# Optimization experiments

Hardware: AMD Instinct MI355X
Metric: run time of the kernel (lower is better)

Reference implementation:

```python
import jax, jax.numpy as jnp
import numpy as np

B, T, E, H, K = 256, 512, 768, 100, 11
START, STOP = 9, 10
NEG = -1000.0


def setup_inputs() -> dict:
    key = jax.random.key(0)
    ks = jax.random.split(key, 12)
    s = 0.1
    Hd = H // 2  # per-direction hidden (bidirectional)
    trans = jax.random.normal(ks[9], (K, K), jnp.float32)
    trans = trans.at[:, START].set(NEG).at[STOP, :].set(NEG)
    return {
        "embeddings": jax.random.normal(ks[0], (B, T, E), jnp.float32),
        "input_mask": jnp.ones((B, T), jnp.int32),
        "W_ih_f": jax.random.normal(ks[1], (4 * Hd, E), jnp.float32) * s,
        "W_hh_f": jax.random.normal(ks[2], (4 * Hd, Hd), jnp.float32) * s,
        "b_f": jax.random.normal(ks[3], (4 * Hd,), jnp.float32) * s,
        "W_ih_b": jax.random.normal(ks[4], (4 * Hd, E), jnp.float32) * s,
        "W_hh_b": jax.random.normal(ks[5], (4 * Hd, Hd), jnp.float32) * s,
        "b_b": jax.random.normal(ks[6], (4 * Hd,), jnp.float32) * s,
        "W_out": jax.random.normal(ks[7], (K, H), jnp.float32) * s,
        "b_out": jax.random.normal(ks[8], (K,), jnp.float32) * s,
        "transitions": trans,
    }


def _lstm_dir(x, W_ih, W_hh, b, reverse):
    # x: [B, T, E] -> hidden states [B, T, Hd]; zero initial state.
    Bn = x.shape[0]
    Hd = W_hh.shape[1]

    def step(carry, xt):
        h, c = carry
        g = xt @ W_ih.T + h @ W_hh.T + b  # [B, 4*Hd], torch gate order i,f,g,o
        i, f, gg, o = jnp.split(g, 4, axis=-1)
        c = jax.nn.sigmoid(f) * c + jax.nn.sigmoid(i) * jnp.tanh(gg)
        h = jax.nn.sigmoid(o) * jnp.tanh(c)
        return (h, c), h

    init = (jnp.zeros((Bn, Hd), x.dtype), jnp.zeros((Bn, Hd), x.dtype))
    _, hs = jax.lax.scan(step, init, jnp.swapaxes(x, 0, 1), reverse=reverse)
    return jnp.swapaxes(hs, 0, 1)


def _emissions(embeddings, W_ih_f, W_hh_f, b_f, W_ih_b, W_hh_b, b_b, W_out, b_out):
    h_f = _lstm_dir(embeddings, W_ih_f, W_hh_f, b_f, reverse=False)
    h_b = _lstm_dir(embeddings, W_ih_b, W_hh_b, b_b, reverse=True)
    lstm_out = jnp.concatenate([h_f, h_b], axis=-1)  # [B, T, H]
    return lstm_out @ W_out.T + b_out  # [B, T, K]


def reference(embeddings, input_mask, W_ih_f, W_hh_f, b_f, W_ih_b, W_hh_b, b_b,
              W_out, b_out, transitions):
    logits = _emissions(embeddings, W_ih_f, W_hh_f, b_f, W_ih_b, W_hh_b, b_b,
                        W_out, b_out)  # [B, T, K]
    Bn = logits.shape[0]
    mask = (input_mask > 0)

    alpha0 = jnp.full((Bn, K), NEG, logits.dtype).at[:, START].set(0.0)
    idK = jnp.arange(K, dtype=jnp.int32)

    def step(alpha, inp):
        frame, m = inp  # frame [B,K], m [B] bool
        # smat[b, prev, cur] = alpha[b,prev] + frame[b,cur] + trans[prev,cur]
        smat = alpha[:, :, None] + frame[:, None, :] + transitions[None]
        bp = jnp.argmax(smat, axis=1).astype(jnp.int32)          # [B, K]
        new_alpha = jax.nn.logsumexp(smat, axis=1)               # [B, K]
        alpha = jnp.where(m[:, None], new_alpha, alpha)
        bp = jnp.where(m[:, None], bp, idK[None, :])
        return alpha, bp

    alpha_T, bps = jax.lax.scan(
        step, alpha0,
        (jnp.swapaxes(logits, 0, 1), jnp.swapaxes(mask, 0, 1)))  # bps [T,B,K]

    final = alpha_T + transitions[None, :, STOP]                 # [B, K]
    scores = jax.nn.logsumexp(final, axis=1)                     # [B]
    best = jnp.argmax(final, axis=1).astype(jnp.int32)           # [B]

    bidx = jnp.arange(Bn)

    def back(cur, bp_t):
        prev = bp_t[bidx, cur]
        return prev, prev

    # Original skips backtrace[0]; backtrack over positions 1..T-1.
    _, path_prefix = jax.lax.scan(back, best, bps[1:], reverse=True)  # [T-1, B]
    paths = jnp.concatenate(
        [jnp.swapaxes(path_prefix, 0, 1), best[:, None]], axis=1)     # [B, T]
    return scores, paths
```

## Files before the change

### kernel.cpp

```cpp
#include <hip/hip_runtime.h>
#include <math.h>


typedef _Float16 half8 __attribute__((ext_vector_type(8)));
typedef _Float16 half4 __attribute__((ext_vector_type(4)));
typedef float f32x4 __attribute__((ext_vector_type(4)));

__global__ __launch_bounds__(256) void k_gemm_split(
    const float* __restrict__ emb,
    const float* __restrict__ Wf,
    const float* __restrict__ Wb,
    float* __restrict__ xw)
{
    __shared__ _Float16 Ah[128 * 64];
    __shared__ _Float16 Al[128 * 64];
    __shared__ _Float16 Bh[80 * 64];
    __shared__ _Float16 Bl[80 * 64];

    const int bid = blockIdx.x;
    const int wg  = (bid & 7) * 640 + (bid >> 3);
    const int mt  = wg / 5;
    const int nb  = wg - mt * 5;
    const size_t m0 = (size_t)mt * 128;
    const int n0 = nb * 80;

    const int tid  = threadIdx.x;
    const int lane = tid & 63;
    const int w    = tid >> 6;
    const int grp  = lane >> 4;
    const int r16  = lane & 15;

    f32x4 acc[2][5];
    #pragma unroll
    for (int m = 0; m < 2; ++m)
        #pragma unroll
        for (int n = 0; n < 5; ++n) acc[m][n] = (f32x4){0.f, 0.f, 0.f, 0.f};

    for (int kt = 0; kt < 12; ++kt) {
        const int k0 = kt * 64;
        __syncthreads();

        #pragma unroll
        for (int j = 0; j < 8; ++j) {
            const int flat = j * 256 + tid;
            const int row  = flat >> 4;
            const int q    = flat & 15;
            const float4 v = *(const float4*)(emb + (m0 + row) * 768 + k0 + q * 4);
            half4 hv, lv;
            hv[0] = (_Float16)v.x; lv[0] = (_Float16)(v.x - (float)hv[0]);
            hv[1] = (_Float16)v.y; lv[1] = (_Float16)(v.y - (float)hv[1]);
            hv[2] = (_Float16)v.z; lv[2] = (_Float16)(v.z - (float)hv[2]);
            hv[3] = (_Float16)v.w; lv[3] = (_Float16)(v.w - (float)hv[3]);
            const int s    = (q >> 1) ^ (row & 7);
            const int addr = row * 64 + s * 8 + (q & 1) * 4;
            *(half4*)(Ah + addr) = hv;
            *(half4*)(Al + addr) = lv;
        }
        #pragma unroll
        for (int j = 0; j < 5; ++j) {
            const int flat = j * 256 + tid;
            const int row  = flat >> 4;
            const int q    = flat & 15;
            const int n    = n0 + row;
            const float* src = (n < 200) ? (Wf + (size_t)n * 768)
                                         : (Wb + (size_t)(n - 200) * 768);
            const float4 v = *(const float4*)(src + k0 + q * 4);
            half4 hv, lv;
            hv[0] = (_Float16)v.x; lv[0] = (_Float16)(v.x - (float)hv[0]);
            hv[1] = (_Float16)v.y; lv[1] = (_Float16)(v.y - (float)hv[1]);
            hv[2] = (_Float16)v.z; lv[2] = (_Float16)(v.z - (float)hv[2]);
            hv[3] = (_Float16)v.w; lv[3] = (_Float16)(v.w - (float)hv[3]);
            const int s    = (q >> 1) ^ (row & 7);
            const int addr = row * 64 + s * 8 + (q & 1) * 4;
            *(half4*)(Bh + addr) = hv;
            *(half4*)(Bl + addr) = lv;
        }
        __syncthreads();

        #pragma unroll
        for (int ks = 0; ks < 2; ++ks) {
            const int kslot = ks * 4 + grp;
            half8 ah[2], al[2], bh[5], bl[5];
            #pragma unroll
            for (int m = 0; m < 2; ++m) {
                const int row = w * 32 + m * 16 + r16;
                const int ad  = row * 64 + (kslot ^ (row & 7)) * 8;
                ah[m] = *(half8*)(Ah + ad);
                al[m] = *(half8*)(Al + ad);
            }
            #pragma unroll
            for (int n = 0; n < 5; ++n) {
                const int row = n * 16 + r16;
                const int ad  = row * 64 + (kslot ^ (row & 7)) * 8;
                bh[n] = *(half8*)(Bh + ad);
                bl[n] = *(half8*)(Bl + ad);
            }
            #pragma unroll
            for (int m = 0; m < 2; ++m)
                #pragma unroll
                for (int n = 0; n < 5; ++n) {
                    acc[m][n] = __builtin_amdgcn_mfma_f32_16x16x32_f16(ah[m], bh[n], acc[m][n], 0, 0, 0);
                    acc[m][n] = __builtin_amdgcn_mfma_f32_16x16x32_f16(ah[m], bl[n], acc[m][n], 0, 0, 0);
                    acc[m][n] = __builtin_amdgcn_mfma_f32_16x16x32_f16(al[m], bh[n], acc[m][n], 0, 0, 0);
                }
        }
    }

    #pragma unroll
    for (int m = 0; m < 2; ++m) {
        #pragma unroll
        for (int n = 0; n < 5; ++n) {
            #pragma unroll
            for (int i = 0; i < 4; ++i) {
                const size_t row = m0 + w * 32 + m * 16 + (lane >> 4) * 4 + i;
                const int    col = n0 + n * 16 + (lane & 15);
                xw[row * 400 + col] = acc[m][n][i];
            }
        }
    }
}

__global__ __launch_bounds__(256) void k_lstm(
    const float* __restrict__ xw,
    const float* __restrict__ Whh_f,
    const float* __restrict__ Whh_b,
    const float* __restrict__ bf_,
    const float* __restrict__ bb_,
    float* __restrict__ hout)
{
    const int b   = blockIdx.x >> 1;
    const int dir = blockIdx.x & 1;
    const int g   = threadIdx.x;

    __shared__ float h_s[52];
    __shared__ float g_s[200];

    const float* Whh  = dir ? Whh_b : Whh_f;
    const float* bias = dir ? bb_ : bf_;

    float w[52];
    float bg = 0.f;
    if (g < 200) {
        #pragma unroll
        for (int j = 0; j < 50; ++j) w[j] = Whh[g * 50 + j];
        w[50] = 0.f; w[51] = 0.f;
        bg = bias[g];
    } else {
        #pragma unroll
        for (int j = 0; j < 52; ++j) w[j] = 0.f;
    }

    if (g < 52) h_s[g] = 0.f;
    float c = 0.f;
    __syncthreads();

    const size_t base = (size_t)b * 512;

    float xv = 0.f;
    {
        int t0 = dir ? 511 : 0;
        if (g < 200) xv = xw[(base + t0) * 400 + dir * 200 + g];
    }

    for (int it = 0; it < 512; ++it) {
        const int t = dir ? (511 - it) : it;
        float xcur = xv;
        if (it + 1 < 512) {
            int tn = dir ? (510 - it) : (it + 1);
            if (g < 200) xv = xw[(base + tn) * 400 + dir * 200 + g];
        }

        float sum = bg + xcur;
        const float4* h4 = (const float4*)h_s;
        #pragma unroll
        for (int q = 0; q < 13; ++q) {
            float4 hv = h4[q];
            sum = fmaf(w[q * 4 + 0], hv.x, sum);
            sum = fmaf(w[q * 4 + 1], hv.y, sum);
            sum = fmaf(w[q * 4 + 2], hv.z, sum);
            sum = fmaf(w[q * 4 + 3], hv.w, sum);
        }
        if (g < 200) g_s[g] = sum;
        __syncthreads();

        if (g < 50) {
            float gi = g_s[g];
            float gf = g_s[g + 50];
            float gg = g_s[g + 100];
            float go = g_s[g + 150];
            float si = 1.f / (1.f + expf(-gi));
            float sf = 1.f / (1.f + expf(-gf));
            float so = 1.f / (1.f + expf(-go));
            c = sf * c + si * tanhf(gg);
            float h = so * tanhf(c);
            hout[(base + t) * 100 + dir * 50 + g] = h;
            h_s[g] = h;
        }
        __syncthreads();
    }
}

__global__ __launch_bounds__(256) void k_emis(
    const float* __restrict__ hout,
    const float* __restrict__ Wout,
    const float* __restrict__ bout,
    float* __restrict__ logits)
{
    __shared__ float Wl[1104];
    __shared__ float bl[11];
    const int tid = threadIdx.x;
    for (int i = tid; i < 1100; i += 256) Wl[i] = Wout[i];
    if (tid < 11) bl[tid] = bout[tid];
    __syncthreads();

    const size_t bt = (size_t)blockIdx.x * 256 + tid;
    const float4* h4 = (const float4*)(hout + bt * 100);
    float acc[11];
    #pragma unroll
    for (int k = 0; k < 11; ++k) acc[k] = bl[k];
    #pragma unroll
    for (int q = 0; q < 25; ++q) {
        float4 v = h4[q];
        #pragma unroll
        for (int k = 0; k < 11; ++k) {
            const float4 wv = *(const float4*)&Wl[k * 100 + q * 4];
            acc[k] = fmaf(v.x, wv.x, fmaf(v.y, wv.y, fmaf(v.z, wv.z, fmaf(v.w, wv.w, acc[k]))));
        }
    }
    #pragma unroll
    for (int k = 0; k < 11; ++k) logits[bt * 11 + k] = acc[k];
}

__global__ __launch_bounds__(64, 1) void k_crf(
    const float* __restrict__ logits,
    const int* __restrict__ mask,
    const float* __restrict__ trans,
    float* __restrict__ scores,
    float* __restrict__ paths)
{
    const int b = blockIdx.x;
    const int lane = threadIdx.x;
    const int lanec = (lane < 11) ? lane : 10;

    __shared__ unsigned char bp[512][12];

    float trc[11], E[11];
    #pragma unroll
    for (int p = 0; p < 11; ++p) {
        trc[p] = trans[p * 11 + lanec];
        E[p]   = expf(trc[p]);
    }

    float al_c = (lane == 9) ? 0.f : -1000.f;

    const size_t lbase = (size_t)b * 512;

    float f_cur = logits[lbase * 11 + lanec];
    int   m_cur = mask[lbase];

    for (int t = 0; t < 512; ++t) {
        float f_next = 0.f; int m_next = 1;
        if (t + 1 < 512) {
            f_next = logits[(lbase + t + 1) * 11 + lanec];
            m_next = mask[lbase + t + 1];
        }

        float a[11];
        #pragma unroll
        for (int p = 0; p < 11; ++p) a[p] = __shfl(al_c, p);

        float vmax = a[0] + trc[0]; int amax = 0;
        #pragma unroll
        for (int p = 1; p < 11; ++p) {
            const float vp = a[p] + trc[p];
            if (vp > vmax) { vmax = vp; amax = p; }
        }

        const float m01 = fmaxf(a[0], a[1]),  m23 = fmaxf(a[2], a[3]);
        const float m45 = fmaxf(a[4], a[5]),  m67 = fmaxf(a[6], a[7]);
        const float m89 = fmaxf(a[8], a[9]);
        const float mA  = fmaxf(fmaxf(m01, m23), fmaxf(m45, m67));
        const float M   = fmaxf(mA, fmaxf(m89, a[10]));

        float e[11];
        #pragma unroll
        for (int p = 0; p < 11; ++p) e[p] = __expf(a[p] - M) * E[p];
        const float s01 = e[0] + e[1], s23 = e[2] + e[3];
        const float s45 = e[4] + e[5], s67 = e[6] + e[7];
        const float s89 = e[8] + e[9];
        const float S = ((s01 + s23) + (s45 + s67)) + (s89 + e[10]);

        const float na = f_cur + (M + __logf(S));

        if (lane < 11) {
            if (m_cur > 0) {
                al_c = na;
                bp[t][lane] = (unsigned char)amax;
            } else {
                bp[t][lane] = (unsigned char)lane;
            }
        }
        f_cur = f_next;
        m_cur = m_next;
    }

    float fin = (lane < 11) ? (al_c + trans[lane * 11 + 10]) : -1e30f;
    float m = fin;
    int am = (lane < 11) ? lane : 1000;
    #pragma unroll
    for (int off = 8; off >= 1; off >>= 1) {
        float om = __shfl_xor(m, off, 16);
        int   oa = __shfl_xor(am, off, 16);
        if (om > m || (om == m && oa < am)) { m = om; am = oa; }
    }
    float s = (lane < 11) ? expf(fin - m) : 0.f;
    #pragma unroll
    for (int off = 8; off >= 1; off >>= 1) s += __shfl_xor(s, off, 16);

    if (lane == 0) {
        scores[b] = m + logf(s);
        int cur = am;
        paths[lbase + 511] = (float)cur;
        for (int t = 511; t >= 1; --t) {
            cur = bp[t][cur];
            paths[lbase + t - 1] = (float)cur;
        }
    }
}

extern "C" void kernel_launch(void* const* d_in, const int* in_sizes, int n_in,
                              void* d_out, int out_size, void* d_ws, size_t ws_size,
                              hipStream_t stream) {
    const float* emb   = (const float*)d_in[0];
    const int*   imask = (const int*)d_in[1];
    const float* Wihf  = (const float*)d_in[2];
    const float* Whhf  = (const float*)d_in[3];
    const float* bf_   = (const float*)d_in[4];
    const float* Wihb  = (const float*)d_in[5];
    const float* Whhb  = (const float*)d_in[6];
    const float* bb_   = (const float*)d_in[7];
    const float* Wout  = (const float*)d_in[8];
    const float* bout  = (const float*)d_in[9];
    const float* trans = (const float*)d_in[10];

    float* out = (float*)d_out;
    float* ws  = (float*)d_ws;
    float* xw     = ws;
    float* hout   = xw + (size_t)131072 * 400;
    float* logits = hout + (size_t)131072 * 100;

    k_gemm_split<<<5120, 256, 0, stream>>>(emb, Wihf, Wihb, xw);
    k_lstm<<<512, 256, 0, stream>>>(xw, Whhf, Whhb, bf_, bb_, hout);
    k_emis<<<512, 256, 0, stream>>>(hout, Wout, bout, logits);
    k_crf<<<256, 64, 0, stream>>>(logits, imask, trans, out, out + 256);
}
```

Measured before the change: 1.004 ms.

## Process two batch sequences per LSTM block to share weights and barriers

Restructures the recurrent LSTM kernel so each block advances two batch elements in the same direction. The per-thread recurrent weight registers and each pair of barriers per step are shared across both sequences. The two gate-activation phases run on separate wavefronts. The launch drops from 512 to 256 blocks, which trades cross-block concurrency on a CU for instruction-level parallelism inside one block.

```diff
diff --git a/kernel.cpp b/kernel.cpp
--- a/kernel.cpp
+++ b/kernel.cpp
@@ -128,12 +128,14 @@
     const float* __restrict__ bb_,
     float* __restrict__ hout)
 {
-    const int b   = blockIdx.x >> 1;
-    const int dir = blockIdx.x & 1;
-    const int g   = threadIdx.x;
-
-    __shared__ float h_s[52];
-    __shared__ float g_s[200];
+    const int pair = blockIdx.x & 127;
+    const int dir  = blockIdx.x >> 7;
+    const int bA   = pair * 2;
+    const int bB   = bA + 1;
+    const int g    = threadIdx.x;
+
+    __shared__ float h_sA[52], h_sB[52];
+    __shared__ float g_sA[200], g_sB[200];
 
     const float* Whh  = dir ? Whh_b : Whh_f;
     const float* bias = dir ? bb_ : bf_;
@@ -150,51 +152,79 @@
         for (int j = 0; j < 52; ++j) w[j] = 0.f;
     }
 
-    if (g < 52) h_s[g] = 0.f;
+    if (g < 52) { h_sA[g] = 0.f; h_sB[g] = 0.f; }
     float c = 0.f;
     __syncthreads();
 
-    const size_t base = (size_t)b * 512;
-
-    float xv = 0.f;
+    const size_t baseA = (size_t)bA * 512;
+    const size_t baseB = (size_t)bB * 512;
+    const int col = dir * 200 + ((g < 200) ? g : 0);
+
+    float xvA = 0.f, xvB = 0.f;
     {
-        int t0 = dir ? 511 : 0;
-        if (g < 200) xv = xw[(base + t0) * 400 + dir * 200 + g];
+        const int t0 = dir ? 511 : 0;
+        if (g < 200) {
+            xvA = xw[(baseA + t0) * 400 + col];
+            xvB = xw[(baseB + t0) * 400 + col];
+        }
     }
 
     for (int it = 0; it < 512; ++it) {
         const int t = dir ? (511 - it) : it;
-        float xcur = xv;
+        const float xcA = xvA, xcB = xvB;
         if (it + 1 < 512) {
-            int tn = dir ? (510 - it) : (it + 1);
-            if (g < 200) xv = xw[(base + tn) * 400 + dir * 200 + g];
-        }
-
-        float sum = bg + xcur;
-        const float4* h4 = (const float4*)h_s;
+            const int tn = dir ? (510 - it) : (it + 1);
+            if (g < 200) {
+                xvA = xw[(baseA + tn) * 400 + col];
+                xvB = xw[(baseB + tn) * 400 + col];
+            }
+        }
+
+        float sumA = bg + xcA;
+        float sumB = bg + xcB;
+        const float4* h4A = (const float4*)h_sA;
+        const float4* h4B = (const float4*)h_sB;
         #pragma unroll
         for (int q = 0; q < 13; ++q) {
-            float4 hv = h4[q];
-            sum = fmaf(w[q * 4 + 0], hv.x, sum);
-            sum = fmaf(w[q * 4 + 1], hv.y, sum);
-            sum = fmaf(w[q * 4 + 2], hv.z, sum);
-            sum = fmaf(w[q * 4 + 3], hv.w, sum);
-        }
-        if (g < 200) g_s[g] = sum;
+            const float4 hvA = h4A[q];
+            const float4 hvB = h4B[q];
+            sumA = fmaf(w[q * 4 + 0], hvA.x, sumA);
+            sumA = fmaf(w[q * 4 + 1], hvA.y, sumA);
+            sumA = fmaf(w[q * 4 + 2], hvA.z, sumA);
+            sumA = fmaf(w[q * 4 + 3], hvA.w, sumA);
+            sumB = fmaf(w[q * 4 + 0], hvB.x, sumB);
+            sumB = fmaf(w[q * 4 + 1], hvB.y, sumB);
+            sumB = fmaf(w[q * 4 + 2], hvB.z, sumB);
+            sumB = fmaf(w[q * 4 + 3], hvB.w, sumB);
+        }
+        if (g < 200) { g_sA[g] = sumA; g_sB[g] = sumB; }
         __syncthreads();
 
         if (g < 50) {
-            float gi = g_s[g];
-            float gf = g_s[g + 50];
-            float gg = g_s[g + 100];
-            float go = g_s[g + 150];
-            float si = 1.f / (1.f + expf(-gi));
-            float sf = 1.f / (1.f + expf(-gf));
-            float so = 1.f / (1.f + expf(-go));
+            const float gi = g_sA[g];
+            const float gf = g_sA[g + 50];
+            const float gg = g_sA[g + 100];
+            const float go = g_sA[g + 150];
+            const float si = 1.f / (1.f + expf(-gi));
+            const float sf = 1.f / (1.f + expf(-gf));
+            const float so = 1.f / (1.f + expf(-go));
             c = sf * c + si * tanhf(gg);
-            float h = so * tanhf(c);
-            hout[(base + t) * 100 + dir * 50 + g] = h;
-            h_s[g] = h;
+            const float h = so * tanhf(c);
+            hout[(baseA + t) * 100 + dir * 50 + g] = h;
+            h_sA[g] = h;
+        } else if (g >= 128 && g < 178) {
+            const int u = g - 128;
+            const float gi = g_sB[u];
+            const float gf = g_sB[u + 50];
+            const float gg = g_sB[u + 100];
+            const float go = g_sB[u + 150];
+            const float si = 1.f / (1.f + expf(-gi));
+            const float sf = 1.f / (1.f + expf(-gf));
+            const float so = 1.f / (1.f + expf(-go));
+            c = sf * c + si * tanhf(gg);
+            const float h = so * tanhf(c);
+            hout[(baseB + t) * 100 + dir * 50 + u] = h;
+            h_sB[u] = h;
         }
         __syncthreads();
     }
@@ -350,7 +380,7 @@
     float* logits = hout + (size_t)131072 * 100;
 
     k_gemm_split<<<5120, 256, 0, stream>>>(emb, Wihf, Wihb, xw);
-    k_lstm<<<512, 256, 0, stream>>>(xw, Whhf, Whhb, bf_, bb_, hout);
+    k_lstm<<<256, 256, 0, stream>>>(xw, Whhf, Whhb, bf_, bb_, hout);
     k_emis<<<512, 256, 0, stream>>>(hout, Wout, bout, logits);
     k_crf<<<256, 64, 0, stream>>>(logits, imask, trans, out, out + 256);
 }
```

Result: slower. 1.085 ms (+8.2%).

## Pre-split input weights to fp16 hi/lo and prefetch next GEMM tile into registers

Applied to the files above, without the earlier changes.

Adds a small kernel that converts the input-projection weights into fp16 high/low halves once, stored in the unused hout workspace. The GEMM then loads ready halves instead of converting weights in every block. The GEMM loop now issues global loads for the next k-tile into registers while the current tile is computed, using barriers that wait only on LDS traffic. This hides global latency and removes redundant conversion work, at the cost of more registers and an extra kernel launch.

```diff
diff --git a/kernel.cpp b/kernel.cpp
--- a/kernel.cpp
+++ b/kernel.cpp
@@ -6,10 +6,34 @@
 typedef _Float16 half4 __attribute__((ext_vector_type(4)));
 typedef float f32x4 __attribute__((ext_vector_type(4)));
 
+#define LBAR() do {                                   \
+    __builtin_amdgcn_sched_barrier(0);                \
+    asm volatile("s_waitcnt lgkmcnt(0)");             \
+    __builtin_amdgcn_s_barrier();                     \
+    __builtin_amdgcn_sched_barrier(0);                \
+} while (0)
+
+__global__ __launch_bounds__(256) void k_bsplit(
+    const float* __restrict__ Wf,
+    const float* __restrict__ Wb,
+    _Float16* __restrict__ Bh,
+    _Float16* __restrict__ Bl)
+{
+    const int i = blockIdx.x * 256 + threadIdx.x;
+    if (i < 400 * 768) {
+        const int n = i / 768;
+        const int k = i - n * 768;
+        const float v = (n < 200) ? Wf[n * 768 + k] : Wb[(n - 200) * 768 + k];
+        const _Float16 hi = (_Float16)v;
+        Bh[i] = hi;
+        Bl[i] = (_Float16)(v - (float)hi);
+    }
+}
+
 __global__ __launch_bounds__(256) void k_gemm_split(
     const float* __restrict__ emb,
-    const float* __restrict__ Wf,
-    const float* __restrict__ Wb,
+    const _Float16* __restrict__ Bhg,
+    const _Float16* __restrict__ Blg,
     float* __restrict__ xw)
 {
     __shared__ _Float16 Ah[128 * 64];
@@ -30,22 +54,44 @@
     const int grp  = lane >> 4;
     const int r16  = lane & 15;
 
+    const int arow = tid >> 1;
+    const int aq0  = (tid & 1) * 8;
+    const int brow = tid >> 4;
+
     f32x4 acc[2][5];
     #pragma unroll
     for (int m = 0; m < 2; ++m)
         #pragma unroll
         for (int n = 0; n < 5; ++n) acc[m][n] = (f32x4){0.f, 0.f, 0.f, 0.f};
 
+    float4 apf[8];
+    half4  bph[5], bpl[5];
+    #pragma unroll
+    for (int j = 0; j < 8; ++j) {
+        const int flat = j * 256 + tid;
+        const int row  = flat >> 4;
+        const int q    = flat & 15;
+        apf[j] = *(const float4*)(emb + (m0 + row) * 768 + q * 4);
+    }
+    #pragma unroll
+    for (int j = 0; j < 5; ++j) {
+        const int flat = j * 256 + tid;
+        const int row  = flat >> 4;
+        const int q    = flat & 15;
+        const size_t src = (size_t)(n0 + row) * 768 + q * 4;
+        bph[j] = *(const half4*)(Bhg + src);
+        bpl[j] = *(const half4*)(Blg + src);
+    }
+
     for (int kt = 0; kt < 12; ++kt) {
-        const int k0 = kt * 64;
-        __syncthreads();
+        LBAR();
 
         #pragma unroll
         for (int j = 0; j < 8; ++j) {
             const int flat = j * 256 + tid;
             const int row  = flat >> 4;
             const int q    = flat & 15;
-            const float4 v = *(const float4*)(emb + (m0 + row) * 768 + k0 + q * 4);
+            const float4 v = apf[j];
             half4 hv, lv;
             hv[0] = (_Float16)v.x; lv[0] = (_Float16)(v.x - (float)hv[0]);
             hv[1] = (_Float16)v.y; lv[1] = (_Float16)(v.y - (float)hv[1]);
@@ -61,21 +107,33 @@
             const int flat = j * 256 + tid;
             const int row  = flat >> 4;
             const int q    = flat & 15;
-            const int n    = n0 + row;
-            const float* src = (n < 200) ? (Wf + (size_t)n * 768)
-                                         : (Wb + (size_t)(n - 200) * 768);
-            const float4 v = *(const float4*)(src + k0 + q * 4);
-            half4 hv, lv;
-            hv[0] = (_Float16)v.x; lv[0] = (_Float16)(v.x - (float)hv[0]);
-            hv[1] = (_Float16)v.y; lv[1] = (_Float16)(v.y - (float)hv[1]);
-            hv[2] = (_Float16)v.z; lv[2] = (_Float16)(v.z - (float)hv[2]);
-            hv[3] = (_Float16)v.w; lv[3] = (_Float16)(v.w - (float)hv[3]);
             const int s    = (q >> 1) ^ (row & 7);
             const int addr = row * 64 + s * 8 + (q & 1) * 4;
-            *(half4*)(Bh + addr) = hv;
-            *(half4*)(Bl + addr) = lv;
-        }
-        __syncthreads();
+            *(half4*)(Bh + addr) = bph[j];
+            *(half4*)(Bl + addr) = bpl[j];
+        }
+
+        if (kt + 1 < 12) {
+            const int k0 = (kt + 1) * 64;
+            #pragma unroll
+            for (int j = 0; j < 8; ++j) {
+                const int flat = j * 256 + tid;
+                const int row  = flat >> 4;
+                const int q    = flat & 15;
+                apf[j] = *(const float4*)(emb + (m0 + row) * 768 + k0 + q * 4);
+            }
+            #pragma unroll
+            for (int j = 0; j < 5; ++j) {
+                const int flat = j * 256 + tid;
+                const int row  = flat >> 4;
+                const int q    = flat & 15;
+                const size_t src = (size_t)(n0 + row) * 768 + k0 + q * 4;
+                bph[j] = *(const half4*)(Bhg + src);
+                bpl[j] = *(const half4*)(Blg + src);
+            }
+        }
+
+        LBAR();
 
         #pragma unroll
         for (int ks = 0; ks < 2; ++ks) {
@@ -349,7 +407,11 @@
     float* hout   = xw + (size_t)131072 * 400;
     float* logits = hout + (size_t)131072 * 100;
 
-    k_gemm_split<<<5120, 256, 0, stream>>>(emb, Wihf, Wihb, xw);
+    _Float16* Bh = (_Float16*)hout;
+    _Float16* Bl = Bh + (size_t)400 * 768;
+
+    k_bsplit<<<1200, 256, 0, stream>>>(Wihf, Wihb, Bh, Bl);
+    k_gemm_split<<<5120, 256, 0, stream>>>(emb, Bh, Bl, xw);
     k_lstm<<<512, 256, 0, stream>>>(xw, Whhf, Whhb, bf_, bb_, hout);
     k_emis<<<512, 256, 0, stream>>>(hout, Wout, bout, logits);
     k_crf<<<256, 64, 0, stream>>>(logits, imask, trans, out, out + 256);
```

Result: faster. 979.3 us (-2.4%).
